# Performance work log

Hardware: AMD Instinct MI355X
Metric: run time of the kernel (lower is better)

The kernel has to match this reference:

```python
import jax, jax.numpy as jnp
import numpy as np

D, H, KV, HD, F = 2048, 16, 4, 128, 5632
WIN, NG = 512, 64          # sliding window size, num global tokens
EPS = 1e-6
KEEP_ATTN = 1.0 - 0.82     # Ramanujan sparsity on attention projections
KEEP_FFN = 1.0 - 0.88      # Ramanujan sparsity on FFN projections


def _mask_w(key, shape, keep):
    """Fixed structured-sparse weight: dense init * binary keep-mask."""
    k1, k2 = jax.random.split(key)
    w = jax.random.normal(k1, shape, dtype=jnp.float32) * (shape[0] ** -0.5)
    m = (jax.random.uniform(k2, shape) < keep).astype(jnp.float32)
    return w * m


def setup_inputs() -> dict:
    key = jax.random.key(0)
    ks = jax.random.split(key, 8)
    x = jax.random.normal(ks[0], (1, 2048, D), dtype=jnp.float32)
    return {
        "x": x,
        "g_attn": jnp.ones((D,), jnp.float32),   # RMSNorm weight (attn)
        "g_ffn": jnp.ones((D,), jnp.float32),    # RMSNorm weight (ffn)
        "wq": _mask_w(ks[1], (D, H * HD), KEEP_ATTN),
        "wk": _mask_w(ks[2], (D, KV * HD), KEEP_ATTN),
        "wv": _mask_w(ks[3], (D, KV * HD), KEEP_ATTN),
        "wo": _mask_w(ks[4], (H * HD, D), KEEP_ATTN),
        "w1": _mask_w(ks[5], (D, F), KEEP_FFN),   # SwiGLU gate proj
        "w3": _mask_w(ks[6], (D, F), KEEP_FFN),   # SwiGLU up proj
        "w2": _mask_w(ks[7], (F, D), KEEP_FFN),   # SwiGLU down proj
    }


def _rmsnorm(x, g):
    return x * jax.lax.rsqrt(jnp.mean(x * x, axis=-1, keepdims=True) + EPS) * g


def _qknorm(t):  # RMS-normalize over head_dim (QK-Normalization)
    return t * jax.lax.rsqrt(jnp.mean(t * t, axis=-1, keepdims=True) + EPS)


def reference(x, g_attn, g_ffn, wq, wk, wv, wo, w1, w2, w3):
    B, S, _ = x.shape
    # --- attention sub-block: x = x + SlidingWindowGQA(RMSNorm(x)) ---
    h = _rmsnorm(x, g_attn)
    q = h @ wq
    q = q.reshape(B, S, H, HD)
    k = (h @ wk).reshape(B, S, KV, HD)
    v = (h @ wv).reshape(B, S, KV, HD)
    q, k = _qknorm(q), _qknorm(k)
    rep = H // KV
    k = jnp.repeat(k, rep, axis=2)  # [B,S,H,HD]
    v = jnp.repeat(v, rep, axis=2)
    scores = jnp.einsum("bihd,bjhd->bhij", q, k) * (HD ** -0.5)
    # causal + (sliding window OR global row OR global column)
    i = jnp.arange(S)[:, None]
    j = jnp.arange(S)[None, :]
    allowed = (j <= i) & (((i - j) < WIN) | (j < NG) | (i < NG))
    scores = jnp.where(allowed[None, None], scores, jnp.float32(-1e30))
    attn = jax.nn.softmax(scores, axis=-1)
    o = jnp.einsum("bhij,bjhd->bihd", attn, v).reshape(B, S, H * HD)
    x = x + o @ wo
    # --- FFN sub-block: x = x + SparseSwiGLU(RMSNorm(x)) ---
    h2 = _rmsnorm(x, g_ffn)
    ffn = (jax.nn.silu(h2 @ w1) * (h2 @ w3)) @ w2
    return x + ffn
```

## Files before the change

kernel.cpp:

```cpp
#include <hip/hip_runtime.h>
#include <hip/hip_bf16.h>
#include <stdint.h>

typedef _Float16 fp16_t;
typedef __attribute__((ext_vector_type(8))) _Float16 fp16x8;
typedef __attribute__((ext_vector_type(4))) _Float16 fp16x4;
typedef __attribute__((ext_vector_type(2))) _Float16 fp16x2;
typedef __attribute__((ext_vector_type(4))) float f32x4;

#define WIN 512
#define NG 64

__device__ __forceinline__ void gload16(const void* g, void* l) {
    __builtin_amdgcn_global_load_lds((const __attribute__((address_space(1))) void*)g,
                                     (__attribute__((address_space(3))) void*)l, 16, 0, 0);
}

__device__ __forceinline__ void tr_tile(const float* __restrict__ src, int C, int srow, int scol,
                                        fp16_t* __restrict__ out, int R, int orow) {
    __shared__ fp16_t t[64][66];
    int tid = threadIdx.x;
    int tx = tid & 15, ty = tid >> 4;
#pragma unroll
    for (int j = 0; j < 4; ++j) {
        int r = ty + j * 16;
        float4 v = *(const float4*)&src[(size_t)(srow + r) * C + scol + tx * 4];
        fp16x2 a = { (fp16_t)v.x, (fp16_t)v.y };
        fp16x2 b = { (fp16_t)v.z, (fp16_t)v.w };
        *(fp16x2*)&t[r][tx * 4] = a;
        *(fp16x2*)&t[r][tx * 4 + 2] = b;
    }
    __syncthreads();
#pragma unroll
    for (int jj = 0; jj < 4; ++jj) {
        int c = ty + jj * 16;
        fp16x4 o = { t[tx * 4 + 0][c], t[tx * 4 + 1][c], t[tx * 4 + 2][c], t[tx * 4 + 3][c] };
        *(fp16x4*)&out[(size_t)(orow + c) * R + srow + tx * 4] = o;
    }
}

__global__ __launch_bounds__(256) void transpose_qkv3(const float* __restrict__ wq,
                                                      const float* __restrict__ wk,
                                                      const float* __restrict__ wv,
                                                      fp16_t* __restrict__ out) {
    int n0 = blockIdx.x * 64, k0 = blockIdx.y * 64;
    const float* src; int C, c0;
    if (n0 < 2048)      { src = wq; C = 2048; c0 = n0; }
    else if (n0 < 2560) { src = wk; C = 512;  c0 = n0 - 2048; }
    else                { src = wv; C = 512;  c0 = n0 - 2560; }
    tr_tile(src, C, k0, c0, out, 2048, n0);
}

__global__ __launch_bounds__(256) void transpose_w13(const float* __restrict__ w1,
                                                     const float* __restrict__ w3,
                                                     fp16_t* __restrict__ o1,
                                                     fp16_t* __restrict__ o3) {
    const float* src = blockIdx.z ? w3 : w1;
    fp16_t* out = blockIdx.z ? o3 : o1;
    tr_tile(src, 5632, blockIdx.y * 64, blockIdx.x * 64, out, 2048, blockIdx.x * 64);
}

__global__ __launch_bounds__(256) void transpose_one(const float* __restrict__ src,
                                                     fp16_t* __restrict__ out, int R, int C) {
    tr_tile(src, C, blockIdx.y * 64, blockIdx.x * 64, out, R, blockIdx.x * 64);
}

__global__ void transpose_b2b(const fp16_t* __restrict__ in, fp16_t* __restrict__ out,
                              int R, int C, int in_ld, int in_off) {
    __shared__ fp16_t t[32][33];
    int tx = threadIdx.x, ty = threadIdx.y;
    int c0 = blockIdx.x * 32, r0 = blockIdx.y * 32;
#pragma unroll
    for (int j = 0; j < 32; j += 8)
        t[ty + j][tx] = in[(size_t)(r0 + ty + j) * in_ld + in_off + c0 + tx];
    __syncthreads();
#pragma unroll
    for (int j = 0; j < 32; j += 8)
        out[(size_t)(c0 + ty + j) * R + r0 + tx] = t[tx][ty + j];
}

__global__ __launch_bounds__(256) void rmsnorm_kernel(const float* __restrict__ in,
                                                      const float* __restrict__ g,
                                                      fp16_t* __restrict__ out) {
    int row = blockIdx.x;
    int tid = threadIdx.x;
    const float4* rp = (const float4*)(in + (size_t)row * 2048);
    float4 v0 = rp[tid], v1 = rp[tid + 256];
    float ss = v0.x * v0.x + v0.y * v0.y + v0.z * v0.z + v0.w * v0.w +
               v1.x * v1.x + v1.y * v1.y + v1.z * v1.z + v1.w * v1.w;
#pragma unroll
    for (int m = 1; m < 64; m <<= 1) ss += __shfl_xor(ss, m);
    __shared__ float red[4];
    if ((tid & 63) == 0) red[tid >> 6] = ss;
    __syncthreads();
    ss = red[0] + red[1] + red[2] + red[3];
    float sc = rsqrtf(ss * (1.0f / 2048.0f) + 1e-6f);
    const float4* gp = (const float4*)g;
    float4 g0 = gp[tid], g1 = gp[tid + 256];
    fp16x4 o0 = { (fp16_t)(v0.x * sc * g0.x), (fp16_t)(v0.y * sc * g0.y),
                  (fp16_t)(v0.z * sc * g0.z), (fp16_t)(v0.w * sc * g0.w) };
    fp16x4 o1 = { (fp16_t)(v1.x * sc * g1.x), (fp16_t)(v1.y * sc * g1.y),
                  (fp16_t)(v1.z * sc * g1.z), (fp16_t)(v1.w * sc * g1.w) };
    *(fp16x4*)(out + (size_t)row * 2048 + tid * 4) = o0;
    *(fp16x4*)(out + (size_t)row * 2048 + 1024 + tid * 4) = o1;
}

__global__ __launch_bounds__(256) void rmsnorm_add2(const float* __restrict__ xin,
                                                    const float* __restrict__ p0,
                                                    const float* __restrict__ p1,
                                                    const float* __restrict__ g,
                                                    float* __restrict__ x1out,
                                                    fp16_t* __restrict__ hout) {
    int row = blockIdx.x;
    int tid = threadIdx.x;
    size_t base = (size_t)row * 2048;
    const float4* xp = (const float4*)(xin + base);
    const float4* ap = (const float4*)(p0 + base);
    const float4* bp = (const float4*)(p1 + base);
    float4 v0 = xp[tid], v1 = xp[tid + 256];
    float4 a0 = ap[tid], a1 = ap[tid + 256];
    float4 b0 = bp[tid], b1 = bp[tid + 256];
    v0.x += a0.x + b0.x; v0.y += a0.y + b0.y; v0.z += a0.z + b0.z; v0.w += a0.w + b0.w;
    v1.x += a1.x + b1.x; v1.y += a1.y + b1.y; v1.z += a1.z + b1.z; v1.w += a1.w + b1.w;
    float ss = v0.x * v0.x + v0.y * v0.y + v0.z * v0.z + v0.w * v0.w +
               v1.x * v1.x + v1.y * v1.y + v1.z * v1.z + v1.w * v1.w;
#pragma unroll
    for (int m = 1; m < 64; m <<= 1) ss += __shfl_xor(ss, m);
    __shared__ float red[4];
    if ((tid & 63) == 0) red[tid >> 6] = ss;
    __syncthreads();
    ss = red[0] + red[1] + red[2] + red[3];
    float sc = rsqrtf(ss * (1.0f / 2048.0f) + 1e-6f);
    ((float4*)(x1out + base))[tid] = v0;
    ((float4*)(x1out + base))[tid + 256] = v1;
    const float4* gp = (const float4*)g;
    float4 g0 = gp[tid], g1 = gp[tid + 256];
    fp16x4 o0 = { (fp16_t)(v0.x * sc * g0.x), (fp16_t)(v0.y * sc * g0.y),
                  (fp16_t)(v0.z * sc * g0.z), (fp16_t)(v0.w * sc * g0.w) };
    fp16x4 o1 = { (fp16_t)(v1.x * sc * g1.x), (fp16_t)(v1.y * sc * g1.y),
                  (fp16_t)(v1.z * sc * g1.z), (fp16_t)(v1.w * sc * g1.w) };
    *(fp16x4*)(hout + base + tid * 4) = o0;
    *(fp16x4*)(hout + base + 1024 + tid * 4) = o1;
}

__global__ __launch_bounds__(256) void final_add2(float* __restrict__ out,
                                                  const float* __restrict__ p0,
                                                  const float* __restrict__ p1) {
    size_t i = (size_t)blockIdx.x * 256 + threadIdx.x;
    float4 o = ((const float4*)out)[i];
    float4 a = ((const float4*)p0)[i];
    float4 b = ((const float4*)p1)[i];
    o.x += a.x + b.x; o.y += a.y + b.y; o.z += a.z + b.z; o.w += a.w + b.w;
    ((float4*)out)[i] = o;
}

#define BM 128
#define BN 128
#define BKK 64

struct GemmCore {
    int tid, lane, wid, lo, hi, wr, wc;
    int arow[4], ascb[4];
    __device__ __forceinline__ void init(int t) {
        tid = t; lane = t & 63; wid = t >> 6;
        lo = lane & 15; hi = lane >> 4;
        wr = (wid >> 1) * 64; wc = (wid & 1) * 64;
#pragma unroll
        for (int p = 0; p < 4; ++p) {
            int idx = (wid * 4 + p) * 64 + lane;
            int row = idx >> 3;
            int cb = (idx & 7) << 4;
            arow[p] = row;
            ascb[p] = cb ^ ((row & 7) << 4);
        }
    }
    __device__ __forceinline__ void stage(char* buf, const fp16_t* A, const fp16_t* Bt,
                                          int brow, int bcol, int lda, int ldb, int kb) {
        char* As = buf;
        char* Bs = buf + 16384;
#pragma unroll
        for (int p = 0; p < 4; ++p) {
            int ci = wid * 4 + p;
            gload16((const char*)A + ((size_t)(brow + arow[p]) * lda + kb) * 2 + ascb[p],
                    As + ci * 1024);
            gload16((const char*)Bt + ((size_t)(bcol + arow[p]) * ldb + kb) * 2 + ascb[p],
                    Bs + ci * 1024);
        }
    }
    __device__ __forceinline__ void compute(const char* buf, f32x4 (&acc)[4][4]) {
        const char* As = buf;
        const char* Bs = buf + 16384;
#pragma unroll
        for (int kc = 0; kc < 2; ++kc) {
            fp16x8 af[4], bfr[4];
            int boff = kc * 64 + hi * 16;
#pragma unroll
            for (int m = 0; m < 4; ++m) {
                int row = wr + m * 16 + lo;
                af[m] = *(const fp16x8*)(As + row * 128 + (boff ^ ((row & 7) << 4)));
            }
#pragma unroll
            for (int n = 0; n < 4; ++n) {
                int row = wc + n * 16 + lo;
                bfr[n] = *(const fp16x8*)(Bs + row * 128 + (boff ^ ((row & 7) << 4)));
            }
#pragma unroll
            for (int m = 0; m < 4; ++m)
#pragma unroll
                for (int n = 0; n < 4; ++n)
                    acc[m][n] = __builtin_amdgcn_mfma_f32_16x16x32_f16(af[m], bfr[n], acc[m][n], 0, 0, 0);
        }
    }
};

template <int EPI>
__global__ __launch_bounds__(256, 2) void gemm_bt(const fp16_t* __restrict__ A,
                                                  const fp16_t* __restrict__ Bt,
                                                  void* __restrict__ Cout,
                                                  const float* __restrict__ resid,
                                                  int M, int N, int K,
                                                  int lda, int ldb, int ksplit) {
    __shared__ __align__(16) char smem[2][32768];
    GemmCore g;
    g.init(threadIdx.x);
    int brow = blockIdx.y * BM, bcol = blockIdx.x * BN;

    int Kloc = K / ksplit;
    int kbase0 = blockIdx.z * Kloc;
    int nK = Kloc / BKK;

    f32x4 acc[4][4] = {};
    g.stage(smem[0], A, Bt, brow, bcol, lda, ldb, kbase0);
    __syncthreads();
    for (int kt = 0; kt < nK; ++kt) {
        if (kt + 1 < nK) g.stage(smem[(kt + 1) & 1], A, Bt, brow, bcol, lda, ldb,
                                 kbase0 + (kt + 1) * BKK);
        g.compute(smem[kt & 1], acc);
        __syncthreads();
    }

    if (EPI == 3) {
        if (blockIdx.x < 20) {
            float* sq = (float*)smem;
            bool isq = blockIdx.x < 16;
#pragma unroll
            for (int m = 0; m < 4; ++m)
#pragma unroll
                for (int r = 0; r < 4; ++r) {
                    float s = 0.f;
#pragma unroll
                    for (int n = 0; n < 4; ++n) s += acc[m][n][r] * acc[m][n][r];
                    s += __shfl_xor(s, 1); s += __shfl_xor(s, 2);
                    s += __shfl_xor(s, 4); s += __shfl_xor(s, 8);
                    if (g.lo == 0) sq[g.wid * 64 + m * 16 + g.hi * 4 + r] = s;
                }
            __syncthreads();
#pragma unroll
            for (int m = 0; m < 4; ++m)
#pragma unroll
                for (int r = 0; r < 4; ++r) {
                    int rl = m * 16 + g.hi * 4 + r;
                    float tot = sq[g.wid * 64 + rl] + sq[(g.wid ^ 1) * 64 + rl];
                    float sc = rsqrtf(tot * (1.0f / 128.0f) + 1e-6f);
                    if (isq) sc *= 0.08838834764831843f;
#pragma unroll
                    for (int n = 0; n < 4; ++n) acc[m][n] [r] *= sc;
                }
        }
    }

#pragma unroll
    for (int m = 0; m < 4; ++m) {
        int grow0 = brow + g.wr + m * 16 + g.hi * 4;
#pragma unroll
        for (int n = 0; n < 4; ++n) {
            int gcol = bcol + g.wc + n * 16 + g.lo;
#pragma unroll
            for (int r = 0; r < 4; ++r) {
                size_t gidx = (size_t)(grow0 + r) * N + gcol;
                float v = acc[m][n][r];
                if (EPI == 0 || EPI == 3) {
                    ((fp16_t*)Cout)[gidx] = (fp16_t)v;
                } else if (EPI == 1) {
                    ((float*)Cout)[gidx] = v + resid[gidx];
                } else {
                    ((float*)Cout)[(size_t)blockIdx.z * M * N + gidx] = v;
                }
            }
        }
    }
}

__global__ __launch_bounds__(256, 2) void gemm_u1u3_fused(const fp16_t* __restrict__ A,
                                                          const fp16_t* __restrict__ Bt1,
                                                          const fp16_t* __restrict__ Bt3,
                                                          fp16_t* __restrict__ G,
                                                          int M, int N, int K) {
    __shared__ __align__(16) char smem[2][32768];
    GemmCore g;
    g.init(threadIdx.x);
    int brow = blockIdx.y * BM, bcol = blockIdx.x * BN;
    int nK = K / BKK;

    f32x4 acc1[4][4] = {}, acc3[4][4] = {};
    g.stage(smem[0], A, Bt1, brow, bcol, K, K, 0);
    __syncthreads();
    for (int kt = 0; kt < nK; ++kt) {
        if (kt + 1 < nK) g.stage(smem[(kt + 1) & 1], A, Bt1, brow, bcol, K, K, (kt + 1) * BKK);
        else             g.stage(smem[(kt + 1) & 1], A, Bt3, brow, bcol, K, K, 0);
        g.compute(smem[kt & 1], acc1);
        __syncthreads();
    }
    for (int kt = 0; kt < nK; ++kt) {
        if (kt + 1 < nK) g.stage(smem[(nK + kt + 1) & 1], A, Bt3, brow, bcol, K, K, (kt + 1) * BKK);
        g.compute(smem[(nK + kt) & 1], acc3);
        __syncthreads();
    }

#pragma unroll
    for (int m = 0; m < 4; ++m) {
        int grow0 = brow + g.wr + m * 16 + g.hi * 4;
#pragma unroll
        for (int n = 0; n < 4; ++n) {
            int gcol = bcol + g.wc + n * 16 + g.lo;
#pragma unroll
            for (int r = 0; r < 4; ++r) {
                float u = acc1[m][n][r];
                float val = (u / (1.0f + __expf(-u))) * acc3[m][n][r];
                G[(size_t)(grow0 + r) * N + gcol] = (fp16_t)val;
            }
        }
    }
}

__global__ __launch_bounds__(256, 2) void attn_kernel(const fp16_t* __restrict__ qkv,
                                                      const fp16_t* __restrict__ vT,
                                                      fp16_t* __restrict__ o) {
    __shared__ __align__(16) char smem[16384 + 16384 + 4 * 2304];
    char* Ks = smem;
    char* VTs = smem + 16384;
    char* Ps = smem + 32768;

    int t = blockIdx.x, qh = blockIdx.y;
    int kvh = qh >> 2;
    int qs = t * 64;
    int tid = threadIdx.x, lane = tid & 63, wid = tid >> 6;
    int lo = lane & 15, hi = lane >> 4;

    fp16x8 qf[4];
    {
        const fp16_t* qptr = qkv + (size_t)(qs + wid * 16 + lo) * 3072 + qh * 128 + hi * 8;
#pragma unroll
        for (int kc = 0; kc < 4; ++kc) qf[kc] = *(const fp16x8*)(qptr + kc * 32);
    }

    f32x4 oacc[8] = {};
    float m_r[4], l_r[4];
#pragma unroll
    for (int r = 0; r < 4; ++r) { m_r[r] = -1e30f; l_r[r] = 0.0f; }

    int lot = qs - (WIN - 1);
    int jt_lo = lot <= 0 ? 0 : (lot >> 6);
    int nt = (jt_lo > 0) ? (t - jt_lo + 2) : (t + 1);

    for (int ti = 0; ti < nt; ++ti) {
        int jt = (jt_lo > 0) ? (ti == 0 ? 0 : jt_lo + ti - 1) : ti;
        int js = jt * 64;
        __syncthreads();
#pragma unroll
        for (int p = 0; p < 4; ++p) {
            int ci = wid * 4 + p;
            int idx = ci * 64 + lane;
            int krow = idx >> 4;
            int kcb = (idx & 15) << 4;
            int kscb = kcb ^ ((krow & 7) << 4);
            gload16((const char*)qkv + ((size_t)(js + krow) * 3072 + 2048 + kvh * 128) * 2 + kscb,
                    Ks + ci * 1024);
            int vrow = idx >> 3;
            int vcb = (idx & 7) << 4;
            int vscb = vcb ^ ((vrow & 7) << 4);
            gload16((const char*)vT + ((size_t)(kvh * 128 + vrow) * 2048 + js) * 2 + vscb,
                    VTs + ci * 1024);
        }
        __syncthreads();

        f32x4 s[4] = {};
#pragma unroll
        for (int kc = 0; kc < 4; ++kc) {
#pragma unroll
            for (int jc = 0; jc < 4; ++jc) {
                int row = jc * 16 + lo;
                fp16x8 kf = *(const fp16x8*)(Ks + row * 256 + ((kc * 64 + hi * 16) ^ ((row & 7) << 4)));
                s[jc] = __builtin_amdgcn_mfma_f32_16x16x32_f16(qf[kc], kf, s[jc], 0, 0, 0);
            }
        }

        float mt[4] = { -1e30f, -1e30f, -1e30f, -1e30f };
#pragma unroll
        for (int jc = 0; jc < 4; ++jc) {
            int j = js + jc * 16 + lo;
#pragma unroll
            for (int r = 0; r < 4; ++r) {
                int i = qs + wid * 16 + hi * 4 + r;
                bool ok = (j <= i) && (((i - j) < WIN) || (j < NG) || (i < NG));
                float sv = ok ? s[jc][r] : -1e30f;
                s[jc][r] = sv;
                mt[r] = fmaxf(mt[r], sv);
            }
        }
#pragma unroll
        for (int m2 = 1; m2 <= 8; m2 <<= 1)
#pragma unroll
            for (int r = 0; r < 4; ++r) mt[r] = fmaxf(mt[r], __shfl_xor(mt[r], m2));
        float sf[4], psum[4];
#pragma unroll
        for (int r = 0; r < 4; ++r) {
            float mn = fmaxf(m_r[r], mt[r]);
            sf[r] = __expf(m_r[r] - mn);
            m_r[r] = mn;
            psum[r] = 0.0f;
        }
#pragma unroll
        for (int jc = 0; jc < 4; ++jc)
#pragma unroll
            for (int r = 0; r < 4; ++r) {
                float p = __expf(s[jc][r] - m_r[r]);
                s[jc][r] = p;
                psum[r] += p;
            }
#pragma unroll
        for (int m2 = 1; m2 <= 8; m2 <<= 1)
#pragma unroll
            for (int r = 0; r < 4; ++r) psum[r] += __shfl_xor(psum[r], m2);
#pragma unroll
        for (int r = 0; r < 4; ++r) l_r[r] = l_r[r] * sf[r] + psum[r];
#pragma unroll
        for (int nc = 0; nc < 8; ++nc)
#pragma unroll
            for (int r = 0; r < 4; ++r) oacc[nc][r] *= sf[r];

        char* Pb = Ps + wid * 2304;
#pragma unroll
        for (int jc = 0; jc < 4; ++jc)
#pragma unroll
            for (int r = 0; r < 4; ++r)
                *(fp16_t*)(Pb + (hi * 4 + r) * 144 + (jc * 16 + lo) * 2) = (fp16_t)s[jc][r];
        fp16x8 pa[2];
#pragma unroll
        for (int jc2 = 0; jc2 < 2; ++jc2)
            pa[jc2] = *(const fp16x8*)(Pb + lo * 144 + jc2 * 64 + hi * 16);

#pragma unroll
        for (int jc2 = 0; jc2 < 2; ++jc2)
#pragma unroll
            for (int nc = 0; nc < 8; ++nc) {
                int row = nc * 16 + lo;
                fp16x8 vf = *(const fp16x8*)(VTs + row * 128 + ((jc2 * 64 + hi * 16) ^ ((row & 7) << 4)));
                oacc[nc] = __builtin_amdgcn_mfma_f32_16x16x32_f16(pa[jc2], vf, oacc[nc], 0, 0, 0);
            }
    }

#pragma unroll
    for (int r = 0; r < 4; ++r) {
        float inv = 1.0f / l_r[r];
        int orow = qs + wid * 16 + hi * 4 + r;
#pragma unroll
        for (int nc = 0; nc < 8; ++nc)
            o[(size_t)orow * 2048 + qh * 128 + nc * 16 + lo] = (fp16_t)(oacc[nc][r] * inv);
    }
}

extern "C" void kernel_launch(void* const* d_in, const int* in_sizes, int n_in,
                              void* d_out, int out_size, void* d_ws, size_t ws_size,
                              hipStream_t stream) {
    const float* x = (const float*)d_in[0];
    const float* g_attn = (const float*)d_in[1];
    const float* g_ffn = (const float*)d_in[2];
    const float* wq = (const float*)d_in[3];
    const float* wk = (const float*)d_in[4];
    const float* wv = (const float*)d_in[5];
    const float* wo = (const float*)d_in[6];
    const float* w1 = (const float*)d_in[7];
    const float* w3 = (const float*)d_in[8];
    const float* w2 = (const float*)d_in[9];
    float* out = (float*)d_out;

    char* ws = (char*)d_ws;
    size_t off = 0;
    auto alloc = [&](size_t bytes) {
        char* p = ws + off;
        off += (bytes + 255) & ~(size_t)255;
        return p;
    };
    fp16_t* hbuf  = (fp16_t*)alloc(2048ull * 2048 * 2);
    fp16_t* wqkvT = (fp16_t*)alloc(3072ull * 2048 * 2);
    fp16_t* vTb   = (fp16_t*)alloc(512ull * 2048 * 2);
    fp16_t* qkv   = (fp16_t*)alloc(2048ull * 3072 * 2);
    fp16_t* gbuf  = (fp16_t*)alloc(2048ull * 5632 * 2);
    float*  part  = (float*)alloc(2ull * 2048 * 2048 * 4);
    fp16_t* wbigT = (fp16_t*)alloc(5632ull * 2048 * 2);
    if (off > ws_size) {
        hipMemsetAsync(d_out, 0, (size_t)out_size * 4, stream);
        return;
    }
    float* part1 = part + 2048ull * 2048;
    fp16_t* w3T = hbuf;

    transpose_qkv3<<<dim3(48, 32), 256, 0, stream>>>(wq, wk, wv, wqkvT);
    rmsnorm_kernel<<<2048, 256, 0, stream>>>(x, g_attn, hbuf);
    gemm_bt<3><<<dim3(24, 16, 1), 256, 0, stream>>>(hbuf, wqkvT, qkv, nullptr,
                                                    2048, 3072, 2048, 2048, 2048, 1);
    transpose_b2b<<<dim3(16, 64), dim3(32, 8), 0, stream>>>(qkv, vTb, 2048, 512, 3072, 2560);
    attn_kernel<<<dim3(32, 16), 256, 0, stream>>>(qkv, vTb, hbuf);
    transpose_one<<<dim3(32, 32), 256, 0, stream>>>(wo, wqkvT, 2048, 2048);
    gemm_bt<2><<<dim3(16, 16, 2), 256, 0, stream>>>(hbuf, wqkvT, part, nullptr,
                                                    2048, 2048, 2048, 2048, 2048, 2);
    rmsnorm_add2<<<2048, 256, 0, stream>>>(x, part, part1, g_ffn, out, qkv);
    transpose_w13<<<dim3(88, 32, 2), 256, 0, stream>>>(w1, w3, wbigT, w3T);
    gemm_u1u3_fused<<<dim3(44, 16), 256, 0, stream>>>(qkv, wbigT, w3T, gbuf, 2048, 5632, 2048);
    transpose_one<<<dim3(32, 88), 256, 0, stream>>>(w2, wbigT, 5632, 2048);
    gemm_bt<2><<<dim3(16, 16, 2), 256, 0, stream>>>(gbuf, wbigT, part, nullptr,
                                                    2048, 2048, 5632, 5632, 5632, 2);
    final_add2<<<4096, 256, 0, stream>>>(out, part, part1);
}
```

Baseline: 323.5 us.

## Fuse V transpose into QKV GEMM epilogue and interleave gate/up GEMM

The QKV GEMM epilogue now writes the V columns straight into the transposed vT buffer, so the separate transpose_b2b kernel and its round trip through memory are gone. The gate/up FFN GEMM is rewritten to load A once per K-step and run the w1 and w3 MFMAs together on a 128x64 tile, instead of reading A twice in two sequential K passes on a 128x128 tile. This doubles the grid to 88x16 blocks and cuts redundant A traffic. In exchange, each block does less compute per A load and the vT stores are 8-byte scattered writes.

```diff
diff --git a/kernel.cpp b/kernel.cpp
--- a/kernel.cpp
+++ b/kernel.cpp
@@ -63,20 +63,6 @@
 __global__ __launch_bounds__(256) void transpose_one(const float* __restrict__ src,
                                                      fp16_t* __restrict__ out, int R, int C) {
     tr_tile(src, C, blockIdx.y * 64, blockIdx.x * 64, out, R, blockIdx.x * 64);
-}
-
-__global__ void transpose_b2b(const fp16_t* __restrict__ in, fp16_t* __restrict__ out,
-                              int R, int C, int in_ld, int in_off) {
-    __shared__ fp16_t t[32][33];
-    int tx = threadIdx.x, ty = threadIdx.y;
-    int c0 = blockIdx.x * 32, r0 = blockIdx.y * 32;
-#pragma unroll
-    for (int j = 0; j < 32; j += 8)
-        t[ty + j][tx] = in[(size_t)(r0 + ty + j) * in_ld + in_off + c0 + tx];
-    __syncthreads();
-#pragma unroll
-    for (int j = 0; j < 32; j += 8)
-        out[(size_t)(c0 + ty + j) * R + r0 + tx] = t[tx][ty + j];
 }
 
 __global__ __launch_bounds__(256) void rmsnorm_kernel(const float* __restrict__ in,
@@ -218,6 +204,7 @@
                                                   const fp16_t* __restrict__ Bt,
                                                   void* __restrict__ Cout,
                                                   const float* __restrict__ resid,
+                                                  fp16_t* __restrict__ vT,
                                                   int M, int N, int K,
                                                   int lda, int ldb, int ksplit) {
     __shared__ __align__(16) char smem[2][32768];
@@ -264,8 +251,21 @@
                     float sc = rsqrtf(tot * (1.0f / 128.0f) + 1e-6f);
                     if (isq) sc *= 0.08838834764831843f;
 #pragma unroll
-                    for (int n = 0; n < 4; ++n) acc[m][n] [r] *= sc;
+                    for (int n = 0; n < 4; ++n) acc[m][n][r] *= sc;
                 }
+        } else {
+#pragma unroll
+            for (int m = 0; m < 4; ++m) {
+                int gcol0 = brow + g.wr + m * 16 + g.hi * 4;
+#pragma unroll
+                for (int n = 0; n < 4; ++n) {
+                    int vrow = bcol + g.wc + n * 16 + g.lo - 2560;
+                    fp16x4 o = { (fp16_t)acc[m][n][0], (fp16_t)acc[m][n][1],
+                                 (fp16_t)acc[m][n][2], (fp16_t)acc[m][n][3] };
+                    *(fp16x4*)&vT[(size_t)vrow * 2048 + gcol0] = o;
+                }
+            }
+            return;
         }
     }
 
@@ -291,38 +291,95 @@
     }
 }
 
-__global__ __launch_bounds__(256, 2) void gemm_u1u3_fused(const fp16_t* __restrict__ A,
-                                                          const fp16_t* __restrict__ Bt1,
-                                                          const fp16_t* __restrict__ Bt3,
-                                                          fp16_t* __restrict__ G,
-                                                          int M, int N, int K) {
+__global__ __launch_bounds__(256, 2) void gemm_u1u3_half(const fp16_t* __restrict__ A,
+                                                         const fp16_t* __restrict__ Bt1,
+                                                         const fp16_t* __restrict__ Bt3,
+                                                         fp16_t* __restrict__ G,
+                                                         int M, int N, int K) {
     __shared__ __align__(16) char smem[2][32768];
-    GemmCore g;
-    g.init(threadIdx.x);
-    int brow = blockIdx.y * BM, bcol = blockIdx.x * BN;
+    int tid = threadIdx.x, lane = tid & 63, wid = tid >> 6;
+    int lo = lane & 15, hi = lane >> 4;
+    int wr = (wid >> 1) * 64, wc = (wid & 1) * 32;
+    int brow = blockIdx.y * 128, bcol = blockIdx.x * 64;
     int nK = K / BKK;
 
-    f32x4 acc1[4][4] = {}, acc3[4][4] = {};
-    g.stage(smem[0], A, Bt1, brow, bcol, K, K, 0);
+    int arow[4], ascb[4];
+#pragma unroll
+    for (int p = 0; p < 4; ++p) {
+        int idx = (wid * 4 + p) * 64 + lane;
+        int row = idx >> 3;
+        int cb = (idx & 7) << 4;
+        arow[p] = row;
+        ascb[p] = cb ^ ((row & 7) << 4);
+    }
+    int brow_[2], bscb[2];
+#pragma unroll
+    for (int p = 0; p < 2; ++p) {
+        int idx = (wid * 2 + p) * 64 + lane;
+        int row = idx >> 3;
+        int cb = (idx & 7) << 4;
+        brow_[p] = row;
+        bscb[p] = cb ^ ((row & 7) << 4);
+    }
+
+    auto stage = [&](char* buf, int kb) {
+        char* As = buf;
+        char* B1s = buf + 16384;
+        char* B3s = buf + 24576;
+#pragma unroll
+        for (int p = 0; p < 4; ++p)
+            gload16((const char*)A + ((size_t)(brow + arow[p]) * K + kb) * 2 + ascb[p],
+                    As + (wid * 4 + p) * 1024);
+#pragma unroll
+        for (int p = 0; p < 2; ++p) {
+            gload16((const char*)Bt1 + ((size_t)(bcol + brow_[p]) * K + kb) * 2 + bscb[p],
+                    B1s + (wid * 2 + p) * 1024);
+            gload16((const char*)Bt3 + ((size_t)(bcol + brow_[p]) * K + kb) * 2 + bscb[p],
+                    B3s + (wid * 2 + p) * 1024);
+        }
+    };
+
+    f32x4 acc1[4][2] = {}, acc3[4][2] = {};
+    stage(smem[0], 0);
     __syncthreads();
     for (int kt = 0; kt < nK; ++kt) {
-        if (kt + 1 < nK) g.stage(smem[(kt + 1) & 1], A, Bt1, brow, bcol, K, K, (kt + 1) * BKK);
-        else             g.stage(smem[(kt + 1) & 1], A, Bt3, brow, bcol, K, K, 0);
-        g.compute(smem[kt & 1], acc1);
+        if (kt + 1 < nK) stage(smem[(kt + 1) & 1], (kt + 1) * BKK);
+        const char* As = smem[kt & 1];
+        const char* B1s = As + 16384;
+        const char* B3s = As + 24576;
+#pragma unroll
+        for (int kc = 0; kc < 2; ++kc) {
+            fp16x8 af[4], b1f[2], b3f[2];
+            int boff = kc * 64 + hi * 16;
+#pragma unroll
+            for (int m = 0; m < 4; ++m) {
+                int row = wr + m * 16 + lo;
+                af[m] = *(const fp16x8*)(As + row * 128 + (boff ^ ((row & 7) << 4)));
+            }
+#pragma unroll
+            for (int n = 0; n < 2; ++n) {
+                int row = wc + n * 16 + lo;
+                int o = row * 128 + (boff ^ ((row & 7) << 4));
+                b1f[n] = *(const fp16x8*)(B1s + o);
+                b3f[n] = *(const fp16x8*)(B3s + o);
+            }
+#pragma unroll
+            for (int m = 0; m < 4; ++m)
+#pragma unroll
+                for (int n = 0; n < 2; ++n) {
+                    acc1[m][n] = __builtin_amdgcn_mfma_f32_16x16x32_f16(af[m], b1f[n], acc1[m][n], 0, 0, 0);
+                    acc3[m][n] = __builtin_amdgcn_mfma_f32_16x16x32_f16(af[m], b3f[n], acc3[m][n], 0, 0, 0);
+                }
+        }
         __syncthreads();
     }
-    for (int kt = 0; kt < nK; ++kt) {
-        if (kt + 1 < nK) g.stage(smem[(nK + kt + 1) & 1], A, Bt3, brow, bcol, K, K, (kt + 1) * BKK);
-        g.compute(smem[(nK + kt) & 1], acc3);
-        __syncthreads();
-    }
 
 #pragma unroll
     for (int m = 0; m < 4; ++m) {
-        int grow0 = brow + g.wr + m * 16 + g.hi * 4;
-#pragma unroll
-        for (int n = 0; n < 4; ++n) {
-            int gcol = bcol + g.wc + n * 16 + g.lo;
+        int grow0 = brow + wr + m * 16 + hi * 4;
+#pragma unroll
+        for (int n = 0; n < 2; ++n) {
+            int gcol = bcol + wc + n * 16 + lo;
 #pragma unroll
             for (int r = 0; r < 4; ++r) {
                 float u = acc1[m][n][r];
@@ -508,18 +565,17 @@
 
     transpose_qkv3<<<dim3(48, 32), 256, 0, stream>>>(wq, wk, wv, wqkvT);
     rmsnorm_kernel<<<2048, 256, 0, stream>>>(x, g_attn, hbuf);
-    gemm_bt<3><<<dim3(24, 16, 1), 256, 0, stream>>>(hbuf, wqkvT, qkv, nullptr,
+    gemm_bt<3><<<dim3(24, 16, 1), 256, 0, stream>>>(hbuf, wqkvT, qkv, nullptr, vTb,
                                                     2048, 3072, 2048, 2048, 2048, 1);
-    transpose_b2b<<<dim3(16, 64), dim3(32, 8), 0, stream>>>(qkv, vTb, 2048, 512, 3072, 2560);
     attn_kernel<<<dim3(32, 16), 256, 0, stream>>>(qkv, vTb, hbuf);
     transpose_one<<<dim3(32, 32), 256, 0, stream>>>(wo, wqkvT, 2048, 2048);
-    gemm_bt<2><<<dim3(16, 16, 2), 256, 0, stream>>>(hbuf, wqkvT, part, nullptr,
+    gemm_bt<2><<<dim3(16, 16, 2), 256, 0, stream>>>(hbuf, wqkvT, part, nullptr, nullptr,
                                                     2048, 2048, 2048, 2048, 2048, 2);
     rmsnorm_add2<<<2048, 256, 0, stream>>>(x, part, part1, g_ffn, out, qkv);
     transpose_w13<<<dim3(88, 32, 2), 256, 0, stream>>>(w1, w3, wbigT, w3T);
-    gemm_u1u3_fused<<<dim3(44, 16), 256, 0, stream>>>(qkv, wbigT, w3T, gbuf, 2048, 5632, 2048);
+    gemm_u1u3_half<<<dim3(88, 16), 256, 0, stream>>>(qkv, wbigT, w3T, gbuf, 2048, 5632, 2048);
     transpose_one<<<dim3(32, 88), 256, 0, stream>>>(w2, wbigT, 5632, 2048);
-    gemm_bt<2><<<dim3(16, 16, 2), 256, 0, stream>>>(gbuf, wbigT, part, nullptr,
+    gemm_bt<2><<<dim3(16, 16, 2), 256, 0, stream>>>(gbuf, wbigT, part, nullptr, nullptr,
                                                     2048, 2048, 5632, 5632, 5632, 2);
     final_add2<<<4096, 256, 0, stream>>>(out, part, part1);
 }
```

Result: faster. 306.6 us (-5.2%).
